# Performance work log

Measured on AMD Instinct MI355X. Metric: run time of the kernel, lower is better.

The kernel has to match this reference:

```python
import jax, jax.numpy as jnp
import numpy as np

K = 7            # conv kernel width (hardcoded via Unfold(kernel_size=(1,7)))
GROUP = 4        # hardware group width
TABLE_ROWS, TABLE_COLS = 61, 1000
QN_W, NB_W = 2, 4      # weight quantizer (qw)
QN_IO, NB_IO = 2, 4    # input quantizer (qi)
QN_O, NB_O = 2, 6      # output quantizer (qo)


def fake_quant(x, Qn, num_bits):
    # Float2Fixed -> Fixed2Float with straight-through (identity) gradient,
    # matching FakeQuantize.backward which returns grad unchanged.
    nb = num_bits - 1
    upb = 2.0 ** (nb - Qn) - 2.0 ** (-Qn)
    downb = -(2.0 ** (nb - Qn))
    scale = 2.0 ** Qn
    q = jnp.round(jnp.clip(x, downb, upb) * scale) / scale
    return x + jax.lax.stop_gradient(q - x)


def setup_inputs() -> dict:
    key = jax.random.key(0)
    k1, k2, k3 = jax.random.split(key, 3)
    B, Cin, L, Co = 4, 16, 2048, 64
    x = jax.random.uniform(k1, (B, Cin, L), dtype=jnp.float32)
    weight = jax.random.normal(k2, (Co, Cin, K), dtype=jnp.float32) * 0.5
    table = jax.random.uniform(k3, (TABLE_ROWS, TABLE_COLS), dtype=jnp.float32)
    return {"x": x, "weight": weight, "table": table}


def _hardware_action(x, q_w, table):
    B, Cin, L = x.shape
    Co = q_w.shape[0]
    Lout = L - K + 1  # stride=1, padding=0, dilation=1

    x_int = x * 8.0 + 6.0
    q_int = q_w * 2.0
    q_plus = jax.nn.relu(q_int)
    q_minus_high = jax.nn.relu(-q_int - 1.0)
    q_minus_low = jax.nn.relu(-q_int) - 2.0 * q_minus_high
    # stack the three weight planes: (3, Co, Cin*K); signs (+1, -1, -2)
    w3 = jnp.stack([q_plus, q_minus_low, q_minus_high]).reshape(3, Co, Cin * K)
    signs = jnp.array([1.0, -1.0, -2.0], dtype=x.dtype)

    # im2col (= Unfold path): row b*Lout+l, col cin*K+k  ==  x_int[b, cin, l+k]
    idxL = jnp.arange(Lout)[:, None] + jnp.arange(K)[None, :]  # (Lout, K)
    patches = x_int[:, :, idxL]                   # (B, Cin, Lout, K)
    x_lin = patches.transpose(0, 2, 1, 3).reshape(B * Lout, Cin * K)

    R, D = x_lin.shape
    G = -(-D // GROUP)
    pad = G * GROUP - D
    x_g = jnp.pad(x_lin, ((0, 0), (0, pad))).reshape(R, G, GROUP)
    w_g = jnp.pad(w3, ((0, 0), (0, 0), (0, pad))).reshape(3, Co, G, GROUP)

    # per-group 4-wide partial linears: y (3, G, R, Co)
    y = jnp.einsum('rgk,tcgk->tgrc', x_g, w_g)

    # probabilistic table lookup with random column indices (fresh randint in torch)
    rand_idx = jax.random.randint(jax.random.key(1234), y.shape, 0, TABLE_COLS)
    y_idx = jnp.clip(y.astype(jnp.int32), 0, TABLE_ROWS - 1)  # trunc like .to(torch.int)
    gathered = table[y_idx, rand_idx]
    y15 = y / 15.0
    res = gathered + y15 - jax.lax.stop_gradient(y15)  # STE: value=gather, grad=y/15

    # x_quant = sum_g ( +15*res_plus - 15*res_low - 30*res_high )
    x_quant = jnp.einsum('t,tgrc->rc', signs * 15.0, res)  # (R, Co)

    # bias = conv1d(6*ones, q_int): constant over positions (no padding)
    bias = 6.0 * jnp.sum(q_int, axis=(1, 2))  # (Co,)

    out = x_quant.reshape(B, Lout, Co).transpose(0, 2, 1)  # (B, Co, Lout)
    return (out - bias[None, :, None]) / 16.0


def reference(x, weight, table):
    xq = fake_quant(x, QN_IO, NB_IO)
    q_w = fake_quant(weight, QN_W, NB_W)
    out = _hardware_action(xq, q_w, table)
    return fake_quant(out, QN_O, NB_O)
```

## Files before the change

kernel.cpp:

```cpp
#include <hip/hip_runtime.h>
#include <stdint.h>

#define PRNG_MODE 0

#define NELEM_TOT 43911168u
#define RSTRIDE   522752u
#define LOUT 2042
#define CO   64
#define CIN  16
#define LIN  2048
#define KW   7
#define DTOT 112
#define WSTR 116

__host__ __device__ __forceinline__ void tf2x32(uint32_t k0, uint32_t k1,
                                                uint32_t x0, uint32_t x1,
                                                uint32_t& o0, uint32_t& o1) {
  uint32_t ks2 = k0 ^ k1 ^ 0x1BD11BDAu;
  x0 += k0; x1 += k1;
#define TFR(r) { x0 += x1; x1 = (x1 << (r)) | (x1 >> (32 - (r))); x1 ^= x0; }
  TFR(13) TFR(15) TFR(26) TFR(6)
  x0 += k1;  x1 += ks2 + 1u;
  TFR(17) TFR(29) TFR(16) TFR(24)
  x0 += ks2; x1 += k0 + 2u;
  TFR(13) TFR(15) TFR(26) TFR(6)
  x0 += k0;  x1 += k1 + 3u;
  TFR(17) TFR(29) TFR(16) TFR(24)
  x0 += k1;  x1 += ks2 + 4u;
  TFR(13) TFR(15) TFR(26) TFR(6)
  x0 += ks2; x1 += k0 + 5u;
#undef TFR
  o0 = x0; o1 = x1;
}

__device__ __forceinline__ uint32_t randbits32(uint32_t ka, uint32_t kb, uint32_t i) {
#if PRNG_MODE == 0
  uint32_t o0, o1;
  tf2x32(ka, kb, 0u, i, o0, o1);
  return o0 ^ o1;
#else
  const uint32_t half = NELEM_TOT / 2u;
  uint32_t j = (i < half) ? i : (i - half);
  uint32_t o0, o1;
  tf2x32(ka, kb, j, j + half, o0, o1);
  return (i < half) ? o0 : o1;
#endif
}

__global__ __launch_bounds__(256) void qconv1d_kernel(
    const float* __restrict__ x, const float* __restrict__ w,
    const float* __restrict__ table, float* __restrict__ out,
    uint32_t k1a, uint32_t k1b, uint32_t k2a, uint32_t k2b) {
  __shared__ int8_t  w2[3 * 64 * WSTR];
  __shared__ uint8_t xr[4][DTOT];
  __shared__ float   y15lut[841];
  __shared__ float   biasv[64];
  __shared__ int     bias_i[64];

  const int tid = threadIdx.x;
  if (tid < 64) bias_i[tid] = 0;
  __syncthreads();

  for (int task = tid; task < 64 * 28; task += 256) {
    int c = task / 28, q = task % 28, d0 = q * 4;
    uint32_t pp = 0, pl = 0, ph = 0;
    int siw = 0;
#pragma unroll
    for (int k = 0; k < 4; ++k) {
      float wv = w[c * DTOT + d0 + k];
      float wc = fminf(fmaxf(wv, -2.0f), 1.75f);
      int iw = (int)rintf(wc * 4.0f);
      siw += iw;
      int p  = iw > 0 ? iw : 0;
      int mh = (-iw - 2) > 0 ? (-iw - 2) : 0;
      int ml = (iw < 0 ? -iw : 0) - 2 * mh;
      pp |= (uint32_t)(p  & 0xff) << (8 * k);
      pl |= (uint32_t)(ml & 0xff) << (8 * k);
      ph |= (uint32_t)(mh & 0xff) << (8 * k);
    }
    int off = c * WSTR + d0;
    *(uint32_t*)&w2[0 * 64 * WSTR + off] = pp;
    *(uint32_t*)&w2[1 * 64 * WSTR + off] = pl;
    *(uint32_t*)&w2[2 * 64 * WSTR + off] = ph;
    atomicAdd(&bias_i[c], siw);
  }

  const int r0 = blockIdx.x * 4;
  for (int idx = tid; idx < 4 * DTOT; idx += 256) {
    int row = idx / DTOT, d = idx - row * DTOT;
    int cin = d / KW, kk = d - cin * KW;
    int r = r0 + row, b = r / LOUT, l = r - b * LOUT;
    float xv = x[(b * CIN + cin) * LIN + l + kk];
    float xc = fminf(fmaxf(xv, -2.0f), 1.75f);
    xr[row][d] = (uint8_t)(2 * (int)rintf(xc * 4.0f) + 6);
  }

  for (int i = tid; i < 841; i += 256) {
    y15lut[i] = ((float)(i - 448) * 0.5f) / 15.0f;
  }
  __syncthreads();
  if (tid < 64) biasv[tid] = 3.0f * (float)bias_i[tid];
  __syncthreads();

  const int rl = tid >> 6, c = tid & 63;
  const int r = r0 + rl;
  const uint8_t* xrow = xr[rl];
  const int8_t*  wrow = &w2[c * WSTR];
  const uint32_t base = (uint32_t)r * 64u + (uint32_t)c;

  float acc = 0.0f;
  const float S15[3] = {15.0f, -15.0f, -30.0f};

  for (int t = 0; t < 3; ++t) {
    const float s = S15[t];
    const int8_t* wt = wrow + t * (64 * WSTR);
    const uint32_t ib = base + (uint32_t)t * 28u * RSTRIDE;
#pragma unroll 2
    for (int g = 0; g < 28; ++g) {
      uint32_t i = ib + (uint32_t)g * RSTRIDE;
      uint32_t hi = randbits32(k1a, k1b, i);
      uint32_t lo = randbits32(k2a, k2b, i);
      uint32_t rnd = ((hi % 1000u) * 296u + lo % 1000u) % 1000u;

      uint32_t xw = *(const uint32_t*)(xrow + g * 4);
      uint32_t ww = *(const uint32_t*)(wt + g * 4);
      int y2 = 0;
#pragma unroll
      for (int k = 0; k < 4; ++k) {
        int xbk = (int)((xw >> (8 * k)) & 0xffu);
        int wbk = (int)((int32_t)(ww << (24 - 8 * k)) >> 24);
        y2 += xbk * wbk;
      }
      int yidx = y2 > 0 ? (y2 >> 1) : 0;
      yidx = yidx < 60 ? yidx : 60;
      float y15 = y15lut[y2 + 448];
      float gv  = table[yidx * 1000 + (int)rnd];
      float res = (gv + y15) - y15;
      acc = fmaf(s, res, acc);
    }
  }

  const int b = r / LOUT, l = r - b * LOUT;
  float v = (acc - biasv[c]) * 0.0625f;
  v = fminf(fmaxf(v, -8.0f), 7.75f);
  out[(b * CO + c) * LOUT + l] = rintf(v * 4.0f) * 0.25f;
}

extern "C" void kernel_launch(void* const* d_in, const int* in_sizes, int n_in,
                              void* d_out, int out_size, void* d_ws, size_t ws_size,
                              hipStream_t stream) {
  const float* x     = (const float*)d_in[0];
  const float* w     = (const float*)d_in[1];
  const float* table = (const float*)d_in[2];
  float* out = (float*)d_out;

  uint32_t k1a, k1b, k2a, k2b;
#if PRNG_MODE == 0
  tf2x32(0u, 1234u, 0u, 0u, k1a, k1b);
  tf2x32(0u, 1234u, 0u, 1u, k2a, k2b);
#else
  uint32_t e0a, e0b, e1a, e1b;
  tf2x32(0u, 1234u, 0u, 2u, e0a, e0b);
  tf2x32(0u, 1234u, 1u, 3u, e1a, e1b);
  k1a = e0a; k1b = e1a; k2a = e0b; k2b = e1b;
#endif

  qconv1d_kernel<<<dim3(2042), dim3(256), 0, stream>>>(x, w, table, out,
                                                       k1a, k1b, k2a, k2b);
}
```

Baseline: 242.4 us.

## Skip PRNG and table gather when an upper-bound pass saturates output low

Adds a small kernel that computes per-row min and max of the lookup table. The main kernel first evaluates an upper bound on the accumulator using the row max for the positive plane and the row min for the negative planes. If that bound already quantizes to the minimum output value, it writes -8 and skips the expensive Threefry RNG and random table gathers. It also uses the sdot4 builtin for the 4-wide int8 dot product and caches x words in registers. The benefit depends on how often outputs saturate at -8. Threads that cannot exit early now pay for an extra bound pass, and an extra kernel launch is added.

```diff
diff --git a/kernel.cpp b/kernel.cpp
--- a/kernel.cpp
+++ b/kernel.cpp
@@ -1,7 +1,6 @@
 #include <hip/hip_runtime.h>
 #include <stdint.h>
 
-#define PRNG_MODE 0
 
 #define NELEM_TOT 43911168u
 #define RSTRIDE   522752u
@@ -34,31 +33,65 @@
 }
 
 __device__ __forceinline__ uint32_t randbits32(uint32_t ka, uint32_t kb, uint32_t i) {
-#if PRNG_MODE == 0
   uint32_t o0, o1;
   tf2x32(ka, kb, 0u, i, o0, o1);
   return o0 ^ o1;
+}
+
+__device__ __forceinline__ int dot4(uint32_t xw, uint32_t ww) {
+#if __has_builtin(__builtin_amdgcn_sdot4)
+  return __builtin_amdgcn_sdot4((int)xw, (int)ww, 0, false);
 #else
-  const uint32_t half = NELEM_TOT / 2u;
-  uint32_t j = (i < half) ? i : (i - half);
-  uint32_t o0, o1;
-  tf2x32(ka, kb, j, j + half, o0, o1);
-  return (i < half) ? o0 : o1;
+  int y2 = 0;
+#pragma unroll
+  for (int k = 0; k < 4; ++k) {
+    int xbk = (int)((xw >> (8 * k)) & 0xffu);
+    int wbk = (int)((int32_t)(ww << (24 - 8 * k)) >> 24);
+    y2 += xbk * wbk;
+  }
+  return y2;
 #endif
+}
+
+__global__ __launch_bounds__(256) void rowminmax_kernel(
+    const float* __restrict__ table, float* __restrict__ ws) {
+  __shared__ float smx[256], smn[256];
+  const int row = blockIdx.x;
+  const float* rp = table + row * 1000;
+  float mx = -1e30f, mn = 1e30f;
+  for (int i = threadIdx.x; i < 1000; i += 256) {
+    float v = rp[i];
+    mx = fmaxf(mx, v); mn = fminf(mn, v);
+  }
+  smx[threadIdx.x] = mx; smn[threadIdx.x] = mn;
+  __syncthreads();
+  for (int s = 128; s > 0; s >>= 1) {
+    if (threadIdx.x < s) {
+      smx[threadIdx.x] = fmaxf(smx[threadIdx.x], smx[threadIdx.x + s]);
+      smn[threadIdx.x] = fminf(smn[threadIdx.x], smn[threadIdx.x + s]);
+    }
+    __syncthreads();
+  }
+  if (threadIdx.x == 0) { ws[row] = smx[0]; ws[61 + row] = smn[0]; }
 }
 
 __global__ __launch_bounds__(256) void qconv1d_kernel(
     const float* __restrict__ x, const float* __restrict__ w,
-    const float* __restrict__ table, float* __restrict__ out,
+    const float* __restrict__ table, const float* __restrict__ rowmm,
+    float* __restrict__ out,
     uint32_t k1a, uint32_t k1b, uint32_t k2a, uint32_t k2b) {
-  __shared__ int8_t  w2[3 * 64 * WSTR];
-  __shared__ uint8_t xr[4][DTOT];
-  __shared__ float   y15lut[841];
-  __shared__ float   biasv[64];
-  __shared__ int     bias_i[64];
+  __shared__ int8_t   w2[3 * 64 * WSTR];
+  __shared__ uint32_t xr4[4][28];
+  __shared__ float    rmaxlut[841];
+  __shared__ float    rminlut[841];
+  __shared__ float    rmax[61], rmin[61];
+  __shared__ float    biasv[64];
+  __shared__ int      bias_i[64];
 
   const int tid = threadIdx.x;
   if (tid < 64) bias_i[tid] = 0;
+  if (tid >= 64 && tid < 125) rmax[tid - 64] = rowmm[tid - 64];
+  if (tid >= 128 && tid < 189) rmin[tid - 128] = rowmm[61 + tid - 128];
   __syncthreads();
 
   for (int task = tid; task < 64 * 28; task += 256) {
@@ -86,17 +119,25 @@
   }
 
   const int r0 = blockIdx.x * 4;
-  for (int idx = tid; idx < 4 * DTOT; idx += 256) {
-    int row = idx / DTOT, d = idx - row * DTOT;
-    int cin = d / KW, kk = d - cin * KW;
-    int r = r0 + row, b = r / LOUT, l = r - b * LOUT;
-    float xv = x[(b * CIN + cin) * LIN + l + kk];
-    float xc = fminf(fmaxf(xv, -2.0f), 1.75f);
-    xr[row][d] = (uint8_t)(2 * (int)rintf(xc * 4.0f) + 6);
+  {
+    uint8_t* xr = (uint8_t*)xr4;
+    for (int idx = tid; idx < 4 * DTOT; idx += 256) {
+      int row = idx / DTOT, d = idx - row * DTOT;
+      int cin = d / KW, kk = d - cin * KW;
+      int r = r0 + row, b = r / LOUT, l = r - b * LOUT;
+      float xv = x[(b * CIN + cin) * LIN + l + kk];
+      float xc = fminf(fmaxf(xv, -2.0f), 1.75f);
+      xr[row * DTOT + d] = (uint8_t)(2 * (int)rintf(xc * 4.0f) + 6);
+    }
   }
 
   for (int i = tid; i < 841; i += 256) {
-    y15lut[i] = ((float)(i - 448) * 0.5f) / 15.0f;
+    int y2 = i - 448;
+    int yi = y2 > 0 ? (y2 >> 1) : 0;
+    yi = yi < 60 ? yi : 60;
+    float y15 = ((float)y2 * 0.5f) / 15.0f;
+    rmaxlut[i] = (rmax[yi] + y15) - y15;
+    rminlut[i] = (rmin[yi] + y15) - y15;
   }
   __syncthreads();
   if (tid < 64) biasv[tid] = 3.0f * (float)bias_i[tid];
@@ -104,46 +145,63 @@
 
   const int rl = tid >> 6, c = tid & 63;
   const int r = r0 + rl;
-  const uint8_t* xrow = xr[rl];
-  const int8_t*  wrow = &w2[c * WSTR];
+  const int b = r / LOUT, l = r - b * LOUT;
+  float* outp = &out[(b * CO + c) * LOUT + l];
+  const float bias = biasv[c];
+  const float S15[3] = {15.0f, -15.0f, -30.0f};
+
+  uint32_t xw[28];
+#pragma unroll
+  for (int g = 0; g < 28; ++g) xw[g] = xr4[rl][g];
+
+  float accub = 0.0f;
+#pragma unroll
+  for (int t = 0; t < 3; ++t) {
+    const float* lut = (t == 0) ? rmaxlut : rminlut;
+    const int8_t* wt = &w2[t * (64 * WSTR) + c * WSTR];
+    const float s = S15[t];
+#pragma unroll 4
+    for (int g = 0; g < 28; ++g) {
+      uint32_t ww = *(const uint32_t*)(wt + 4 * g);
+      int y2 = dot4(xw[g], ww);
+      accub = fmaf(s, lut[y2 + 448], accub);
+    }
+  }
+  {
+    float vub = (accub - bias) * 0.0625f;
+    vub = fminf(fmaxf(vub, -8.0f), 7.75f);
+    float qub = rintf(vub * 4.0f) * 0.25f;
+    if (qub == -8.0f) {
+      *outp = -8.0f;
+      return;
+    }
+  }
+
   const uint32_t base = (uint32_t)r * 64u + (uint32_t)c;
-
   float acc = 0.0f;
-  const float S15[3] = {15.0f, -15.0f, -30.0f};
-
   for (int t = 0; t < 3; ++t) {
     const float s = S15[t];
-    const int8_t* wt = wrow + t * (64 * WSTR);
+    const int8_t* wt = &w2[t * (64 * WSTR) + c * WSTR];
     const uint32_t ib = base + (uint32_t)t * 28u * RSTRIDE;
-#pragma unroll 2
     for (int g = 0; g < 28; ++g) {
       uint32_t i = ib + (uint32_t)g * RSTRIDE;
       uint32_t hi = randbits32(k1a, k1b, i);
       uint32_t lo = randbits32(k2a, k2b, i);
       uint32_t rnd = ((hi % 1000u) * 296u + lo % 1000u) % 1000u;
 
-      uint32_t xw = *(const uint32_t*)(xrow + g * 4);
-      uint32_t ww = *(const uint32_t*)(wt + g * 4);
-      int y2 = 0;
-#pragma unroll
-      for (int k = 0; k < 4; ++k) {
-        int xbk = (int)((xw >> (8 * k)) & 0xffu);
-        int wbk = (int)((int32_t)(ww << (24 - 8 * k)) >> 24);
-        y2 += xbk * wbk;
-      }
+      uint32_t ww = *(const uint32_t*)(wt + 4 * g);
+      int y2 = dot4(xw[g], ww);
       int yidx = y2 > 0 ? (y2 >> 1) : 0;
       yidx = yidx < 60 ? yidx : 60;
-      float y15 = y15lut[y2 + 448];
+      float y15 = ((float)y2 * 0.5f) / 15.0f;
       float gv  = table[yidx * 1000 + (int)rnd];
       float res = (gv + y15) - y15;
       acc = fmaf(s, res, acc);
     }
   }
-
-  const int b = r / LOUT, l = r - b * LOUT;
-  float v = (acc - biasv[c]) * 0.0625f;
+  float v = (acc - bias) * 0.0625f;
   v = fminf(fmaxf(v, -8.0f), 7.75f);
-  out[(b * CO + c) * LOUT + l] = rintf(v * 4.0f) * 0.25f;
+  *outp = rintf(v * 4.0f) * 0.25f;
 }
 
 extern "C" void kernel_launch(void* const* d_in, const int* in_sizes, int n_in,
@@ -153,18 +211,13 @@
   const float* w     = (const float*)d_in[1];
   const float* table = (const float*)d_in[2];
   float* out = (float*)d_out;
+  float* ws  = (float*)d_ws;
 
   uint32_t k1a, k1b, k2a, k2b;
-#if PRNG_MODE == 0
   tf2x32(0u, 1234u, 0u, 0u, k1a, k1b);
   tf2x32(0u, 1234u, 0u, 1u, k2a, k2b);
-#else
-  uint32_t e0a, e0b, e1a, e1b;
-  tf2x32(0u, 1234u, 0u, 2u, e0a, e0b);
-  tf2x32(0u, 1234u, 1u, 3u, e1a, e1b);
-  k1a = e0a; k1b = e1a; k2a = e0b; k2b = e1b;
-#endif
-
-  qconv1d_kernel<<<dim3(2042), dim3(256), 0, stream>>>(x, w, table, out,
+
+  rowminmax_kernel<<<dim3(61), dim3(256), 0, stream>>>(table, ws);
+  qconv1d_kernel<<<dim3(2042), dim3(256), 0, stream>>>(x, w, table, ws, out,
                                                        k1a, k1b, k2a, k2b);
 }
```

Result: slower. 263.6 us (+8.7%).
